# Kernel tuning notes

Hardware: AMD Instinct MI355X
Metric: run time of the kernel (lower is better)

## Reference

```python
import jax, jax.numpy as jnp
import numpy as np

Q_DIM = 1024
CTX_DIM = 1024
HEADS = 16
DIM_HEAD = 64
INNER = HEADS * DIM_HEAD  # 1024
MLP_HIDDEN = int(4.0 * Q_DIM)
EPS = 1e-5


def layer_norm(x, g, b):
    mu = jnp.mean(x, axis=-1, keepdims=True)
    var = jnp.var(x, axis=-1, keepdims=True)
    return (x - mu) * jax.lax.rsqrt(var + EPS) * g + b


def setup_inputs() -> dict:
    key = jax.random.key(0)
    ks = jax.random.split(key, 12)
    s = 0.02
    return {
        "x": jax.random.normal(ks[0], (4, 2048, Q_DIM), jnp.float32),
        "context": jax.random.normal(ks[1], (4, 2048, CTX_DIM), jnp.float32),
        # attention projections (stored [in, out])
        "Wq": jax.random.normal(ks[2], (Q_DIM, INNER), jnp.float32) * s,
        "Wk": jax.random.normal(ks[3], (CTX_DIM, INNER), jnp.float32) * s,
        "Wv": jax.random.normal(ks[4], (CTX_DIM, INNER), jnp.float32) * s,
        "Wo": jax.random.normal(ks[5], (INNER, Q_DIM), jnp.float32) * s,
        "bo": jnp.zeros((Q_DIM,), jnp.float32),
        # layer norms
        "g_q": jnp.ones((Q_DIM,), jnp.float32), "b_q": jnp.zeros((Q_DIM,), jnp.float32),
        "g_k": jnp.ones((CTX_DIM,), jnp.float32), "b_k": jnp.zeros((CTX_DIM,), jnp.float32),
        "g_m": jnp.ones((Q_DIM,), jnp.float32), "b_m": jnp.zeros((Q_DIM,), jnp.float32),
        # mlp
        "W1": jax.random.normal(ks[6], (Q_DIM, MLP_HIDDEN), jnp.float32) * s,
        "b1": jnp.zeros((MLP_HIDDEN,), jnp.float32),
        "W2": jax.random.normal(ks[7], (MLP_HIDDEN, Q_DIM), jnp.float32) * s,
        "b2": jnp.zeros((Q_DIM,), jnp.float32),
    }


def reference(x, context, Wq, Wk, Wv, Wo, bo, g_q, b_q, g_k, b_k, g_m, b_m, W1, b1, W2, b2):
    B, N, _ = x.shape
    M = context.shape[1]
    scale = DIM_HEAD ** -0.5

    xn = layer_norm(x, g_q, b_q)
    cn = layer_norm(context, g_k, b_k)

    # project and split heads: [B, H, N, D]
    q = (xn @ Wq).reshape(B, N, HEADS, DIM_HEAD).transpose(0, 2, 1, 3)
    k = (cn @ Wk).reshape(B, M, HEADS, DIM_HEAD).transpose(0, 2, 1, 3)
    v = (cn @ Wv).reshape(B, M, HEADS, DIM_HEAD).transpose(0, 2, 1, 3)

    sim = jnp.einsum('bhid,bhjd->bhij', q, k) * scale  # [B,H,N,M]
    attn = jax.nn.softmax(sim, axis=-1)
    out = jnp.einsum('bhij,bhjd->bhid', attn, v)        # [B,H,N,D]
    out = out.transpose(0, 2, 1, 3).reshape(B, N, INNER)
    x = x + out @ Wo + bo

    h = layer_norm(x, g_m, b_m)
    h = jax.nn.silu(h @ W1 + b1) @ W2 + b2
    return x + h
```

## Files before the change

### kernel.cpp

```cpp
#include <hip/hip_runtime.h>
#include <hip/hip_bf16.h>


typedef __bf16 bf16x8 __attribute__((ext_vector_type(8)));
typedef __bf16 bf16x4 __attribute__((ext_vector_type(4)));
typedef float f32x4 __attribute__((ext_vector_type(4)));

#define DEV static __device__ __forceinline__

DEV short f2bf(float x) {
  union { float f; unsigned u; } c; c.f = x;
  unsigned r = c.u + 0x7fffu + ((c.u >> 16) & 1u);
  return (short)(r >> 16);
}

DEV void gload_lds16(const void* g, void* l) {
  __builtin_amdgcn_global_load_lds((__attribute__((address_space(1))) void*)g,
                                   (__attribute__((address_space(3))) void*)l, 16, 0, 0);
}

__launch_bounds__(256, 4)
__global__ void transpose_f32_bf16(const float* __restrict__ in, short* __restrict__ outT,
                                   int R, int C) {
  __shared__ float t[32][33];
  const int c0 = blockIdx.x * 32, r0 = blockIdx.y * 32;
  const int tx = threadIdx.x, ty = threadIdx.y;
#pragma unroll
  for (int i = 0; i < 4; ++i)
    t[ty + 8 * i][tx] = in[(size_t)(r0 + ty + 8 * i) * C + (c0 + tx)];
  __syncthreads();
#pragma unroll
  for (int i = 0; i < 4; ++i)
    outT[(size_t)(c0 + ty + 8 * i) * R + (r0 + tx)] = f2bf(t[tx][ty + 8 * i]);
}

__launch_bounds__(256, 4)
__global__ void transpose_v(const short* __restrict__ KV, short* __restrict__ Vt) {
  __shared__ short t[32][33];
  const int m0 = blockIdx.x * 32;
  const int d0 = blockIdx.y * 32;
  const int bh = blockIdx.z;
  const int b = bh >> 4, h = bh & 15;
  const int tx = threadIdx.x, ty = threadIdx.y;
#pragma unroll
  for (int i = 0; i < 4; ++i)
    t[ty + 8 * i][tx] = KV[((size_t)b * 2048 + m0 + ty + 8 * i) * 2048 + 1024 + h * 64 + d0 + tx];
  __syncthreads();
#pragma unroll
  for (int i = 0; i < 4; ++i)
    Vt[((size_t)bh * 64 + d0 + ty + 8 * i) * 2048 + (m0 + tx)] = t[tx][ty + 8 * i];
}

__launch_bounds__(256, 4)
__global__ void ln_kernel(const float* __restrict__ in, const float* __restrict__ g,
                          const float* __restrict__ b, short* __restrict__ out) {
  const int row = blockIdx.x;
  const int tid = threadIdx.x;
  const float4 v = ((const float4*)(in + (size_t)row * 1024))[tid];
  float s = v.x + v.y + v.z + v.w;
  float s2 = v.x * v.x + v.y * v.y + v.z * v.z + v.w * v.w;
#pragma unroll
  for (int off = 1; off < 64; off <<= 1) {
    s += __shfl_xor(s, off);
    s2 += __shfl_xor(s2, off);
  }
  __shared__ float ps[4], pq[4];
  const int w = tid >> 6, lane = tid & 63;
  if (lane == 0) { ps[w] = s; pq[w] = s2; }
  __syncthreads();
  s = ps[0] + ps[1] + ps[2] + ps[3];
  s2 = pq[0] + pq[1] + pq[2] + pq[3];
  const float mu = s * (1.f / 1024.f);
  const float rs = rsqrtf(s2 * (1.f / 1024.f) - mu * mu + 1e-5f);
  const float4 gg = ((const float4*)g)[tid];
  const float4 bb = ((const float4*)b)[tid];
  short4 o4;
  o4.x = f2bf((v.x - mu) * rs * gg.x + bb.x);
  o4.y = f2bf((v.y - mu) * rs * gg.y + bb.y);
  o4.z = f2bf((v.z - mu) * rs * gg.z + bb.z);
  o4.w = f2bf((v.w - mu) * rs * gg.w + bb.w);
  ((short4*)(out + (size_t)row * 1024))[tid] = o4;
}

enum { EPI_Q = 0, EPI_PLAIN = 1, EPI_BIAS_RESID_F32 = 2, EPI_BIAS_SILU = 3, EPI_PARTIAL = 4 };

DEV void epi_store(int EPI, size_t idx, int cg, float v, const float* bias,
                   const float* resid, float scale, short* outb, float* outf) {
  if (EPI == EPI_Q) {
    outb[idx] = f2bf(v * scale);
  } else if (EPI == EPI_PLAIN) {
    outb[idx] = f2bf(v);
  } else if (EPI == EPI_BIAS_RESID_F32) {
    outf[idx] = v + bias[cg] + resid[idx];
  } else if (EPI == EPI_BIAS_SILU) {
    const float u = v + bias[cg];
    outb[idx] = f2bf(u / (1.f + __expf(-u)));
  } else {
    outf[idx] = v;
  }
}

template <int EPI>
DEV void gemm_core(const short* __restrict__ A, const short* __restrict__ Bt,
                   int lda, int ldb, int k0, int nit, int N, int nbx, int nwg, int id,
                   const float* __restrict__ bias, const float* __restrict__ resid,
                   float scale, short* __restrict__ outb, float* __restrict__ outf,
                   char* Albase, char* Blbase) {
  const int tid = threadIdx.x;
  const int lane = tid & 63, w = tid >> 6;
  const int wr = w >> 2, wc = w & 3;
  const int lg = lane >> 4, lr = lane & 15;
  const int swz = (id & 7) * (nwg >> 3) + (id >> 3);
  const int bx = swz % nbx, by = swz / nbx;
  const int row0 = by * 256, col0 = bx * 256;
  const int rsw = (lr & 7) << 4;
  const int scb = (((tid & 7) ^ ((tid >> 3) & 7)) << 4);
  const size_t lda2 = (size_t)lda * 2, ldb2 = (size_t)ldb * 2;
  const char* Asrc = (const char*)A + (size_t)(row0 + (tid >> 3)) * lda2 + (size_t)k0 * 2 + scb;
  const char* Bsrc = (const char*)Bt + (size_t)(col0 + (tid >> 3)) * ldb2 + (size_t)k0 * 2 + scb;
  char* Adst = Albase + w * 1024;
  char* Bdst = Blbase + w * 1024;

#define STG_A(t, h) do { \
    gload_lds16(Asrc + (size_t)((h) * 128) * lda2 + (size_t)(t) * 128, \
                Adst + (((t) & 1) * 2 + (h)) * 16384); \
    gload_lds16(Asrc + (size_t)((h) * 128 + 64) * lda2 + (size_t)(t) * 128, \
                Adst + (((t) & 1) * 2 + (h)) * 16384 + 8192); } while (0)
#define STG_B(t, h) do { \
    gload_lds16(Bsrc + (size_t)((h) * 128) * ldb2 + (size_t)(t) * 128, \
                Bdst + (((t) & 1) * 2 + (h)) * 16384); \
    gload_lds16(Bsrc + (size_t)((h) * 128 + 64) * ldb2 + (size_t)(t) * 128, \
                Bdst + (((t) & 1) * 2 + (h)) * 16384 + 8192); } while (0)
#define RD_A(buf, mq, mi, ks) (*(const bf16x8*)(Albase + ((buf) * 2 + wr) * 16384 + \
    ((mq) * 64 + (mi) * 16 + lr) * 128 + (((ks) * 64 + lg * 16) ^ rsw)))
#define RD_B(buf, nq, ni, ks) (*(const bf16x8*)(Blbase + ((buf) * 2 + (wc >> 1)) * 16384 + \
    ((wc & 1) * 64 + (nq) * 32 + (ni) * 16 + lr) * 128 + (((ks) * 64 + lg * 16) ^ rsw)))
#define MFMA_Q(mq, nq, BF) do { \
    __builtin_amdgcn_s_setprio(1); \
    _Pragma("unroll") for (int mi_ = 0; mi_ < 4; ++mi_) \
    _Pragma("unroll") for (int ni_ = 0; ni_ < 2; ++ni_) \
    _Pragma("unroll") for (int ks_ = 0; ks_ < 2; ++ks_) \
      acc[(mq) * 4 + mi_][(nq) * 2 + ni_] = __builtin_amdgcn_mfma_f32_16x16x32_bf16( \
          af[mi_][ks_], BF[ni_][ks_], acc[(mq) * 4 + mi_][(nq) * 2 + ni_], 0, 0, 0); \
    __builtin_amdgcn_s_setprio(0); } while (0)
#define PH_ENTRY() do { __builtin_amdgcn_sched_barrier(0); __builtin_amdgcn_s_barrier(); \
    __builtin_amdgcn_sched_barrier(0); } while (0)
#define PH_LGKM() do { asm volatile("s_waitcnt lgkmcnt(0)" ::: "memory"); \
    __builtin_amdgcn_sched_barrier(0); } while (0)

  STG_B(0, 0); STG_B(0, 1); STG_A(0, 0); STG_A(0, 1);
  STG_B(1, 0); STG_B(1, 1); STG_A(1, 0); STG_A(1, 1);

  f32x4 acc[8][4] = {};
  bf16x8 af[4][2], b0[2][2], b1[2][2];

#pragma unroll 1
  for (int i = 0; i < nit; ++i) {
    const int t2 = 2 * i + 2, t3 = 2 * i + 3;
    const bool pf = (i + 1 < nit);
    asm volatile("s_waitcnt vmcnt(8)" ::: "memory");
    PH_ENTRY();
#pragma unroll
    for (int mi = 0; mi < 4; ++mi) { af[mi][0] = RD_A(0, 0, mi, 0); af[mi][1] = RD_A(0, 0, mi, 1); }
#pragma unroll
    for (int ni = 0; ni < 2; ++ni) { b0[ni][0] = RD_B(0, 0, ni, 0); b0[ni][1] = RD_B(0, 0, ni, 1); }
    PH_LGKM();
    MFMA_Q(0, 0, b0);
    PH_ENTRY();
#pragma unroll
    for (int ni = 0; ni < 2; ++ni) { b1[ni][0] = RD_B(0, 1, ni, 0); b1[ni][1] = RD_B(0, 1, ni, 1); }
    PH_LGKM();
    MFMA_Q(0, 1, b1);
    PH_ENTRY();
#pragma unroll
    for (int mi = 0; mi < 4; ++mi) { af[mi][0] = RD_A(0, 1, mi, 0); af[mi][1] = RD_A(0, 1, mi, 1); }
    if (pf) { STG_B(t2, 0); STG_B(t2, 1); }
    PH_LGKM();
    MFMA_Q(1, 0, b0);
    PH_ENTRY();
    if (pf) { STG_A(t2, 0); STG_A(t2, 1); }
    PH_LGKM();
    MFMA_Q(1, 1, b1);
    if (pf) asm volatile("s_waitcnt vmcnt(8)" ::: "memory");
    else    asm volatile("s_waitcnt vmcnt(0)" ::: "memory");
    PH_ENTRY();
#pragma unroll
    for (int mi = 0; mi < 4; ++mi) { af[mi][0] = RD_A(1, 0, mi, 0); af[mi][1] = RD_A(1, 0, mi, 1); }
#pragma unroll
    for (int ni = 0; ni < 2; ++ni) { b0[ni][0] = RD_B(1, 0, ni, 0); b0[ni][1] = RD_B(1, 0, ni, 1); }
    PH_LGKM();
    MFMA_Q(0, 0, b0);
    PH_ENTRY();
#pragma unroll
    for (int ni = 0; ni < 2; ++ni) { b1[ni][0] = RD_B(1, 1, ni, 0); b1[ni][1] = RD_B(1, 1, ni, 1); }
    PH_LGKM();
    MFMA_Q(0, 1, b1);
    PH_ENTRY();
#pragma unroll
    for (int mi = 0; mi < 4; ++mi) { af[mi][0] = RD_A(1, 1, mi, 0); af[mi][1] = RD_A(1, 1, mi, 1); }
    if (pf) { STG_B(t3, 0); STG_B(t3, 1); }
    PH_LGKM();
    MFMA_Q(1, 0, b0);
    PH_ENTRY();
    if (pf) { STG_A(t3, 0); STG_A(t3, 1); }
    PH_LGKM();
    MFMA_Q(1, 1, b1);
  }
#undef STG_A
#undef STG_B
#undef RD_A
#undef RD_B
#undef MFMA_Q
#undef PH_ENTRY
#undef PH_LGKM
#pragma unroll
  for (int mi = 0; mi < 8; ++mi) {
#pragma unroll
    for (int nj = 0; nj < 4; ++nj) {
      const int cg = col0 + wc * 64 + (nj >> 1) * 32 + (nj & 1) * 16 + lr;
#pragma unroll
      for (int r = 0; r < 4; ++r) {
        const int rg = row0 + wr * 128 + (mi >> 2) * 64 + (mi & 3) * 16 + lg * 4 + r;
        epi_store(EPI, (size_t)rg * N + cg, cg, acc[mi][nj][r], bias, resid, scale, outb, outf);
      }
    }
  }
}

template <int EPI>
__launch_bounds__(512, 2)
__global__ void gemm256k(const short* __restrict__ A, const short* __restrict__ Bt,
                         int lda, int ldb, int ksub, int N, int nbx,
                         const float* __restrict__ bias, const float* __restrict__ resid,
                         float scale, short* __restrict__ outb, float* __restrict__ outf) {
  __shared__ short Al[2][2][128 * 64];
  __shared__ short Bl[2][2][128 * 64];
  const int k0 = blockIdx.y * ksub;
  float* of = outf;
  if (EPI == EPI_PARTIAL) of = outf + (size_t)blockIdx.y * 8192 * 1024;
  gemm_core<EPI>(A, Bt, lda, ldb, k0, ksub >> 7, N, nbx, gridDim.x, blockIdx.x,
                 bias, resid, scale, outb, of, (char*)&Al[0][0][0], (char*)&Bl[0][0][0]);
}

__launch_bounds__(256, 8)
__global__ void splitk_reduce(const float* __restrict__ p0, const float* __restrict__ p1,
                              const float* __restrict__ bias, const float* __restrict__ resid,
                              float* __restrict__ out) {
  const size_t i = (size_t)blockIdx.x * 256 + threadIdx.x;
  const int col4 = (int)(i & 255);
  const float4 a = ((const float4*)p0)[i];
  const float4 b = ((const float4*)p1)[i];
  const float4 c = ((const float4*)resid)[i];
  const float4 g = ((const float4*)bias)[col4];
  float4 o;
  o.x = a.x + b.x + c.x + g.x;
  o.y = a.y + b.y + c.y + g.y;
  o.z = a.z + b.z + c.z + g.z;
  o.w = a.w + b.w + c.w + g.w;
  ((float4*)out)[i] = o;
}

__launch_bounds__(512, 4)
__global__ void attn_kernel(const short* __restrict__ Qg, const short* __restrict__ KVg,
                            const short* __restrict__ Vtg, short* __restrict__ AO) {
  __shared__ short Kl[2][64 * 64];
  __shared__ short Vl[2][64 * 64];
  __shared__ short Pl[8][32 * 64];
  const int tid = threadIdx.x;
  const int lane = tid & 63, w = tid >> 6;
  const int lg = lane >> 4, lr = lane & 15;

  const int id = blockIdx.x;
  const int xcd = id & 7, j = id >> 3;
  const int bh = xcd * 8 + (j & 7);
  const int qblk = j >> 3;
  const int b = bh >> 4, h = bh & 15;
  const int q0 = qblk * 256 + w * 32;

  bf16x8 qf[2][2];
#pragma unroll
  for (int qb = 0; qb < 2; ++qb) {
    const short* qp = Qg + ((size_t)b * 2048 + q0 + qb * 16 + lr) * 1024 + h * 64 + lg * 8;
    qf[qb][0] = *(const bf16x8*)qp;
    qf[qb][1] = *(const bf16x8*)(qp + 32);
  }

  const int srow = lane >> 3;
  const int scb = ((lane & 7) << 4) ^ (srow << 4);
  const char* Ks = (const char*)KVg + ((size_t)b * 2048 + w * 8 + srow) * 4096 + h * 128 + scb;
  const char* Vs = (const char*)Vtg + ((size_t)bh * 64 + w * 8 + srow) * 4096 + scb;
  char* KB[2] = {(char*)&Kl[0][0] + w * 1024, (char*)&Kl[1][0] + w * 1024};
  char* VB[2] = {(char*)&Vl[0][0] + w * 1024, (char*)&Vl[1][0] + w * 1024};

  f32x4 acc[2][4] = {};
  float m_run[2] = {-1e30f, -1e30f};
  float l_run[2] = {0.f, 0.f};
  char* Pw = (char*)&Pl[w][0];
  const int sw = (lr & 7) << 4;

  gload_lds16(Ks, KB[0]);
  gload_lds16(Vs, VB[0]);
  __syncthreads();
  int buf = 0;

  for (int kv0 = 0; kv0 < 2048; kv0 += 64) {
    if (kv0 + 64 < 2048) {
      gload_lds16(Ks + (size_t)(kv0 + 64) * 4096, KB[buf ^ 1]);
      gload_lds16(Vs + (size_t)(kv0 + 64) * 2, VB[buf ^ 1]);
    }
    f32x4 st[4][2];
#pragma unroll
    for (int t = 0; t < 4; ++t) {
      const char* kb = (const char*)&Kl[buf][0] + (t * 16 + lr) * 128;
      const bf16x8 kf0 = *(const bf16x8*)(kb + ((lg * 16) ^ sw));
      const bf16x8 kf1 = *(const bf16x8*)(kb + ((64 + lg * 16) ^ sw));
#pragma unroll
      for (int qb = 0; qb < 2; ++qb) {
        f32x4 z = {};
        z = __builtin_amdgcn_mfma_f32_16x16x32_bf16(kf0, qf[qb][0], z, 0, 0, 0);
        z = __builtin_amdgcn_mfma_f32_16x16x32_bf16(kf1, qf[qb][1], z, 0, 0, 0);
        st[t][qb] = z;
      }
    }
#pragma unroll
    for (int qb = 0; qb < 2; ++qb) {
      float smax = st[0][qb][0];
#pragma unroll
      for (int t = 0; t < 4; ++t)
#pragma unroll
        for (int r = 0; r < 4; ++r) smax = fmaxf(smax, st[t][qb][r]);
      smax = fmaxf(smax, __shfl_xor(smax, 16));
      smax = fmaxf(smax, __shfl_xor(smax, 32));
      float m_use = m_run[qb];
      if (!__all(smax - m_use <= 8.f)) {
        const float mnew = fmaxf(m_use, smax);
        const float alpha = __builtin_amdgcn_exp2f(m_use - mnew);
        m_run[qb] = mnew;
        m_use = mnew;
        l_run[qb] *= alpha;
        float ar[4];
#pragma unroll
        for (int r = 0; r < 4; ++r) ar[r] = __shfl(alpha, lg * 4 + r);
#pragma unroll
        for (int dt = 0; dt < 4; ++dt)
#pragma unroll
          for (int r = 0; r < 4; ++r) acc[qb][dt][r] *= ar[r];
      }
      float rsum = 0.f;
#pragma unroll
      for (int t = 0; t < 4; ++t) {
        bf16x4 pk;
        float ps = 0.f;
#pragma unroll
        for (int r = 0; r < 4; ++r) {
          const float p = __builtin_amdgcn_exp2f(st[t][qb][r] - m_use);
          ps += p;
          pk[r] = (__bf16)p;
        }
        rsum += ps;
        *(bf16x4*)(Pw + (qb * 16 + lr) * 128 + ((t * 32 + lg * 8) ^ sw)) = pk;
      }
      rsum += __shfl_xor(rsum, 16);
      rsum += __shfl_xor(rsum, 32);
      l_run[qb] += rsum;
    }
#pragma unroll
    for (int c = 0; c < 2; ++c) {
      const bf16x8 pf0 = *(const bf16x8*)(Pw + lr * 128 + ((c * 64 + lg * 16) ^ sw));
      const bf16x8 pf1 = *(const bf16x8*)(Pw + (16 + lr) * 128 + ((c * 64 + lg * 16) ^ sw));
#pragma unroll
      for (int dt = 0; dt < 4; ++dt) {
        const bf16x8 vf = *(const bf16x8*)((const char*)&Vl[buf][0] + (dt * 16 + lr) * 128 +
                                           ((c * 64 + lg * 16) ^ sw));
        acc[0][dt] = __builtin_amdgcn_mfma_f32_16x16x32_bf16(pf0, vf, acc[0][dt], 0, 0, 0);
        acc[1][dt] = __builtin_amdgcn_mfma_f32_16x16x32_bf16(pf1, vf, acc[1][dt], 0, 0, 0);
      }
    }
    __syncthreads();
    buf ^= 1;
  }
#pragma unroll
  for (int qb = 0; qb < 2; ++qb) {
    const float linv = 1.f / l_run[qb];
    float lv[4];
#pragma unroll
    for (int r = 0; r < 4; ++r) lv[r] = __shfl(linv, lg * 4 + r);
#pragma unroll
    for (int dt = 0; dt < 4; ++dt)
#pragma unroll
      for (int r = 0; r < 4; ++r)
        AO[((size_t)b * 2048 + q0 + qb * 16 + lg * 4 + r) * 1024 + h * 64 + dt * 16 + lr] =
            f2bf(acc[qb][dt][r] * lv[r]);
  }
}

extern "C" void kernel_launch(void* const* d_in, const int* in_sizes, int n_in,
                              void* d_out, int out_size, void* d_ws, size_t ws_size,
                              hipStream_t stream) {
  const float* x   = (const float*)d_in[0];
  const float* ctx = (const float*)d_in[1];
  const float* Wq  = (const float*)d_in[2];
  const float* Wk  = (const float*)d_in[3];
  const float* Wv  = (const float*)d_in[4];
  const float* Wo  = (const float*)d_in[5];
  const float* bo  = (const float*)d_in[6];
  const float* g_q = (const float*)d_in[7];
  const float* b_q = (const float*)d_in[8];
  const float* g_k = (const float*)d_in[9];
  const float* b_k = (const float*)d_in[10];
  const float* g_m = (const float*)d_in[11];
  const float* b_m = (const float*)d_in[12];
  const float* W1  = (const float*)d_in[13];
  const float* b1  = (const float*)d_in[14];
  const float* W2  = (const float*)d_in[15];
  const float* b2  = (const float*)d_in[16];
  float* out = (float*)d_out;

  short* p = (short*)d_ws;
  short* xn   = p; p += (size_t)8192 * 1024;
  short* cn   = p; p += (size_t)8192 * 1024;
  short* Qb   = p; p += (size_t)8192 * 1024;
  short* KVb  = p; p += (size_t)8192 * 2048;
  short* Vts  = p; p += (size_t)8192 * 1024;
  short* AO   = p; p += (size_t)8192 * 1024;
  short* hn   = p; p += (size_t)8192 * 1024;
  short* hm   = p; p += (size_t)8192 * 4096;
  short* WqT  = p; p += (size_t)1024 * 1024;
  short* WkvT = p; p += (size_t)2048 * 1024;
  short* WoT  = p; p += (size_t)1024 * 1024;
  short* W1T  = p; p += (size_t)1024 * 4096;
  short* W2T  = p; p += (size_t)4096 * 1024;
  float* x2   = (float*)p;
  float* part = (float*)Qb;

  const dim3 tb(32, 8);
  transpose_f32_bf16<<<dim3(32, 32), tb, 0, stream>>>(Wq, WqT, 1024, 1024);
  transpose_f32_bf16<<<dim3(32, 32), tb, 0, stream>>>(Wk, WkvT, 1024, 1024);
  transpose_f32_bf16<<<dim3(32, 32), tb, 0, stream>>>(Wv, WkvT + (size_t)1024 * 1024, 1024, 1024);
  transpose_f32_bf16<<<dim3(32, 32), tb, 0, stream>>>(Wo, WoT, 1024, 1024);
  transpose_f32_bf16<<<dim3(128, 32), tb, 0, stream>>>(W1, W1T, 1024, 4096);
  transpose_f32_bf16<<<dim3(32, 128), tb, 0, stream>>>(W2, W2T, 4096, 1024);

  ln_kernel<<<8192, 256, 0, stream>>>(x, g_q, b_q, xn);
  ln_kernel<<<8192, 256, 0, stream>>>(ctx, g_k, b_k, cn);

  const float qscale = 0.125f * 1.44269504088896340736f;
  gemm256k<EPI_Q><<<dim3(128, 1), 512, 0, stream>>>(xn, WqT, 1024, 1024, 1024, 1024, 4,
                                                    nullptr, nullptr, qscale, Qb, nullptr);
  gemm256k<EPI_PLAIN><<<dim3(256, 1), 512, 0, stream>>>(cn, WkvT, 1024, 1024, 1024, 2048, 8,
                                                        nullptr, nullptr, 0.f, KVb, nullptr);

  transpose_v<<<dim3(64, 2, 64), tb, 0, stream>>>(KVb, Vts);

  attn_kernel<<<512, 512, 0, stream>>>(Qb, KVb, Vts, AO);

  gemm256k<EPI_BIAS_RESID_F32><<<dim3(128, 1), 512, 0, stream>>>(AO, WoT, 1024, 1024, 1024, 1024, 4,
                                                                 bo, x, 0.f, nullptr, x2);

  ln_kernel<<<8192, 256, 0, stream>>>(x2, g_m, b_m, hn);

  gemm256k<EPI_BIAS_SILU><<<dim3(512, 1), 512, 0, stream>>>(hn, W1T, 1024, 1024, 1024, 4096, 16,
                                                            b1, nullptr, 0.f, hm, nullptr);
  gemm256k<EPI_PARTIAL><<<dim3(128, 2), 512, 0, stream>>>(hm, W2T, 4096, 4096, 2048, 1024, 4,
                                                          nullptr, nullptr, 0.f, nullptr, part);
  splitk_reduce<<<8192, 256, 0, stream>>>(part, part + (size_t)8192 * 1024, b2, x2, out);
}
```

Measured before the change: 432.5 us.

## Restructure GEMM phase barriers into mid/post pairs around MFMA clusters

Reorganizes the 8-wave ping-pong GEMM main loop so each phase has a barrier before and after its MFMA cluster, with the LDS wait placed after the first barrier. The vmcnt wait for the next tile moves to just after issuing the last prefetch, and an initial wait plus barrier is hoisted before the loop. The aim is to let waves interleave LDS reads and MFMA work across the workgroup more evenly, in the style of ping-pong scheduling. It adds one extra barrier per phase, which can cost time if the waves do not overlap as intended.

Measured after the change: 448.5 us. 3.7% more time.

```diff
diff --git a/kernel.cpp b/kernel.cpp
--- a/kernel.cpp
+++ b/kernel.cpp
@@ -143,13 +143,18 @@
       acc[(mq) * 4 + mi_][(nq) * 2 + ni_] = __builtin_amdgcn_mfma_f32_16x16x32_bf16( \
           af[mi_][ks_], BF[ni_][ks_], acc[(mq) * 4 + mi_][(nq) * 2 + ni_], 0, 0, 0); \
     __builtin_amdgcn_s_setprio(0); } while (0)
-#define PH_ENTRY() do { __builtin_amdgcn_sched_barrier(0); __builtin_amdgcn_s_barrier(); \
+#define PH_MID() do { __builtin_amdgcn_sched_barrier(0); __builtin_amdgcn_s_barrier(); \
+    asm volatile("s_waitcnt lgkmcnt(0)" ::: "memory"); \
     __builtin_amdgcn_sched_barrier(0); } while (0)
-#define PH_LGKM() do { asm volatile("s_waitcnt lgkmcnt(0)" ::: "memory"); \
+#define PH_POST() do { __builtin_amdgcn_sched_barrier(0); __builtin_amdgcn_s_barrier(); \
     __builtin_amdgcn_sched_barrier(0); } while (0)
 
   STG_B(0, 0); STG_B(0, 1); STG_A(0, 0); STG_A(0, 1);
   STG_B(1, 0); STG_B(1, 1); STG_A(1, 0); STG_A(1, 1);
+  asm volatile("s_waitcnt vmcnt(8)" ::: "memory");
+  __builtin_amdgcn_sched_barrier(0);
+  __builtin_amdgcn_s_barrier();
+  __builtin_amdgcn_sched_barrier(0);
 
   f32x4 acc[8][4] = {};
   bf16x8 af[4][2], b0[2][2], b1[2][2];
@@ -158,61 +163,66 @@
   for (int i = 0; i < nit; ++i) {
     const int t2 = 2 * i + 2, t3 = 2 * i + 3;
     const bool pf = (i + 1 < nit);
-    asm volatile("s_waitcnt vmcnt(8)" ::: "memory");
-    PH_ENTRY();
 #pragma unroll
     for (int mi = 0; mi < 4; ++mi) { af[mi][0] = RD_A(0, 0, mi, 0); af[mi][1] = RD_A(0, 0, mi, 1); }
 #pragma unroll
     for (int ni = 0; ni < 2; ++ni) { b0[ni][0] = RD_B(0, 0, ni, 0); b0[ni][1] = RD_B(0, 0, ni, 1); }
-    PH_LGKM();
+    PH_MID();
     MFMA_Q(0, 0, b0);
-    PH_ENTRY();
+    PH_POST();
 #pragma unroll
     for (int ni = 0; ni < 2; ++ni) { b1[ni][0] = RD_B(0, 1, ni, 0); b1[ni][1] = RD_B(0, 1, ni, 1); }
-    PH_LGKM();
+    PH_MID();
     MFMA_Q(0, 1, b1);
-    PH_ENTRY();
+    PH_POST();
 #pragma unroll
     for (int mi = 0; mi < 4; ++mi) { af[mi][0] = RD_A(0, 1, mi, 0); af[mi][1] = RD_A(0, 1, mi, 1); }
     if (pf) { STG_B(t2, 0); STG_B(t2, 1); }
-    PH_LGKM();
+    PH_MID();
     MFMA_Q(1, 0, b0);
-    PH_ENTRY();
-    if (pf) { STG_A(t2, 0); STG_A(t2, 1); }
-    PH_LGKM();
+    PH_POST();
+    if (pf) {
+      STG_A(t2, 0); STG_A(t2, 1);
+      asm volatile("s_waitcnt vmcnt(8)" ::: "memory");
+    } else {
+      asm volatile("s_waitcnt vmcnt(0)" ::: "memory");
+    }
+    PH_MID();
     MFMA_Q(1, 1, b1);
-    if (pf) asm volatile("s_waitcnt vmcnt(8)" ::: "memory");
-    else    asm volatile("s_waitcnt vmcnt(0)" ::: "memory");
-    PH_ENTRY();
+    PH_POST();
 #pragma unroll
     for (int mi = 0; mi < 4; ++mi) { af[mi][0] = RD_A(1, 0, mi, 0); af[mi][1] = RD_A(1, 0, mi, 1); }
 #pragma unroll
     for (int ni = 0; ni < 2; ++ni) { b0[ni][0] = RD_B(1, 0, ni, 0); b0[ni][1] = RD_B(1, 0, ni, 1); }
-    PH_LGKM();
+    PH_MID();
     MFMA_Q(0, 0, b0);
-    PH_ENTRY();
+    PH_POST();
 #pragma unroll
     for (int ni = 0; ni < 2; ++ni) { b1[ni][0] = RD_B(1, 1, ni, 0); b1[ni][1] = RD_B(1, 1, ni, 1); }
-    PH_LGKM();
+    PH_MID();
     MFMA_Q(0, 1, b1);
-    PH_ENTRY();
+    PH_POST();
 #pragma unroll
     for (int mi = 0; mi < 4; ++mi) { af[mi][0] = RD_A(1, 1, mi, 0); af[mi][1] = RD_A(1, 1, mi, 1); }
     if (pf) { STG_B(t3, 0); STG_B(t3, 1); }
-    PH_LGKM();
+    PH_MID();
     MFMA_Q(1, 0, b0);
-    PH_ENTRY();
-    if (pf) { STG_A(t3, 0); STG_A(t3, 1); }
-    PH_LGKM();
+    PH_POST();
+    if (pf) {
+      STG_A(t3, 0); STG_A(t3, 1);
+      asm volatile("s_waitcnt vmcnt(8)" ::: "memory");
+    }
+    PH_MID();
     MFMA_Q(1, 1, b1);
+    PH_POST();
   }
 #undef STG_A
 #undef STG_B
 #undef RD_A
 #undef RD_B
 #undef MFMA_Q
-#undef PH_ENTRY
-#undef PH_LGKM
+#undef PH_MID
+#undef PH_POST
 #pragma unroll
   for (int mi = 0; mi < 8; ++mi) {
 #pragma unroll
```
